# Performance work log

Hardware: AMD Instinct MI355X
Metric: run time of the kernel (lower is better)

The kernel has to match this reference:

```python
import jax, jax.numpy as jnp
import numpy as np
import math

D_MODEL = 1024
N_HEADS = 8
HEAD_DIM = D_MODEL // N_HEADS
N_CLASSES = 2


def setup_inputs() -> dict:
    key = jax.random.key(0)
    ks = jax.random.split(key, 12)
    s = 1.0 / math.sqrt(D_MODEL)
    return {
        "x": jax.random.normal(ks[0], (8192, D_MODEL), dtype=jnp.float32),
        "class_token": jax.random.normal(ks[1], (1, 1, D_MODEL), dtype=jnp.float32),
        "Wq": jax.random.normal(ks[2], (D_MODEL, D_MODEL), dtype=jnp.float32) * s,
        "bq": jnp.zeros((D_MODEL,), jnp.float32),
        "Wk": jax.random.normal(ks[3], (D_MODEL, D_MODEL), dtype=jnp.float32) * s,
        "bk": jnp.zeros((D_MODEL,), jnp.float32),
        "Wv": jax.random.normal(ks[4], (D_MODEL, D_MODEL), dtype=jnp.float32) * s,
        "bv": jnp.zeros((D_MODEL,), jnp.float32),
        "Wo": jax.random.normal(ks[5], (D_MODEL, D_MODEL), dtype=jnp.float32) * s,
        "bo": jnp.zeros((D_MODEL,), jnp.float32),
        "Wc": jax.random.normal(ks[6], (N_CLASSES, D_MODEL), dtype=jnp.float32) * s,
        "bc": jnp.zeros((N_CLASSES,), jnp.float32),
    }


def reference(x, class_token, Wq, bq, Wk, bk, Wv, bv, Wo, bo, Wc, bc):
    # Prepend class token: [T, D] with T = N_patches + 1 (batch size is 1)
    tokens = jnp.concatenate([class_token.reshape(1, D_MODEL), x], axis=0)
    T = tokens.shape[0]
    scale = 1.0 / math.sqrt(HEAD_DIM)

    def heads(W, b):
        return (tokens @ W.T + b).reshape(T, N_HEADS, HEAD_DIM).transpose(1, 0, 2)

    q = heads(Wq, bq)  # [H, T, hd]
    k = heads(Wk, bk)
    v = heads(Wv, bv)

    scores = jnp.einsum("htd,hsd->hts", q, k) * scale  # [H, T, T]
    probs = jax.nn.softmax(scores, axis=-1)
    attn_out = jnp.einsum("hts,hsd->htd", probs, v)  # [H, T, hd]

    # MIL attention weights: class-token row, over patches, head-averaged
    A = probs[:, 0, 1:].mean(axis=0)[None, :]  # [1, N_patches]

    out = attn_out.transpose(1, 0, 2).reshape(T, D_MODEL) @ Wo.T + bo  # [T, D]
    cls_out = out[0:1]  # [1, D]

    logits = cls_out @ Wc.T + bc  # [1, n_classes]
    y_probs = jax.nn.softmax(logits, axis=1)

    m = jnp.argmax(y_probs.reshape(-1))
    row = m // N_CLASSES
    Y_hat = (m % N_CLASSES)[None]  # [1]
    top_instance = jnp.take(logits, row, axis=0)[None]  # [1, n_classes]
    Y_prob = jnp.take(y_probs, row, axis=0)[None]  # [1, n_classes]

    return top_instance, Y_prob, Y_hat, y_probs, A
```

## Files before the change

### kernel.cpp

```cpp
#include <hip/hip_runtime.h>
#include <math.h>

#define D 1024
#define NH 8
#define T 8193

#define OFF_LOGITS 0
#define OFF_DONE   2
#define OFF_E      4
#define OFF_G      2052
#define OFF_W      18436
#define ZERO_FLTS  26628
#define OFF_QCLS   26628
#define OFF_CH     27652
#define OFF_CONST  27660
#define OFF_L      27664
#define OFF_SCT    29712
#define OFF_UB     95256

static __device__ __forceinline__ float wred(float v) {
    #pragma unroll
    for (int m = 32; m; m >>= 1) v += __shfl_xor(v, m, 64);
    return v;
}

#define DPPADD(v, ctrl) \
    ((v) + __int_as_float(__builtin_amdgcn_update_dpp( \
        0, __float_as_int(v), (ctrl), 0xf, 0xf, true)))

static __device__ __forceinline__ float wave_total(float v) {
    v = DPPADD(v, 0x111);
    v = DPPADD(v, 0x112);
    v = DPPADD(v, 0x114);
    v = DPPADD(v, 0x118);
    v = DPPADD(v, 0x142);
    v = DPPADD(v, 0x143);
    return __int_as_float(__builtin_amdgcn_readlane(__float_as_int(v), 63));
}

__global__ __launch_bounds__(256) void k1(const float* __restrict__ Wq,
                                          const float* __restrict__ bq,
                                          const float* __restrict__ ct,
                                          const float* __restrict__ Wc,
                                          const float* __restrict__ Wo,
                                          float* __restrict__ ws) {
    __shared__ float red[4];
    int b = blockIdx.x, t = threadIdx.x;
    if (b < 1024) {
        const float4* wr = (const float4*)(Wq + (size_t)b * D);
        const float4* cv = (const float4*)ct;
        float4 a = wr[t], c = cv[t];
        float v = a.x*c.x + a.y*c.y + a.z*c.z + a.w*c.w;
        v = wred(v);
        if ((t & 63) == 0) red[t >> 6] = v;
        __syncthreads();
        if (t == 0) ws[OFF_QCLS + b] = red[0]+red[1]+red[2]+red[3] + bq[b];
    } else {
        int idx = b - 1024;
        int c = idx >> 5, i0 = (idx & 31) * 32;
        const float4* Wo4 = (const float4*)Wo;
        float4 acc = {0,0,0,0};
        #pragma unroll 8
        for (int i = 0; i < 32; ++i) {
            float s = Wc[c * D + i0 + i];
            float4 r = Wo4[(size_t)(i0 + i) * 256 + t];
            acc.x += s*r.x; acc.y += s*r.y; acc.z += s*r.z; acc.w += s*r.w;
        }
        float* e = ws + OFF_E + c * D + t * 4;
        atomicAdd(e+0, acc.x); atomicAdd(e+1, acc.y);
        atomicAdd(e+2, acc.z); atomicAdd(e+3, acc.w);
    }
}

__global__ __launch_bounds__(1024) void k2(const float* __restrict__ Wk,
                                           const float* __restrict__ bk,
                                           const float* __restrict__ Wv,
                                           const float* __restrict__ Wc,
                                           const float* __restrict__ bo,
                                           const float* __restrict__ bv,
                                           const float* __restrict__ bc,
                                           float* __restrict__ ws) {
    int b = blockIdx.x, t = threadIdx.x;
    int w = t >> 6, lane = t & 63;
    if (b < 64) {
        int h = b >> 3, seg = b & 7;
        float acc = 0.f;
        const float* base = Wk + ((size_t)(h*128 + seg*16)) * D + t;
        #pragma unroll
        for (int d = 0; d < 16; ++d)
            acc += ws[OFF_QCLS + h*128 + seg*16 + d] * base[(size_t)d * D];
        atomicAdd(&ws[OFF_W + h*D + t], acc);
    } else if (b < 192) {
        __shared__ float4 gred[4][256];
        int idx = b - 64;
        int c = idx >> 6, h = (idx >> 3) & 7, rseg = idx & 7;
        int j4 = t & 255, rsub = t >> 8;
        int r0 = h*128 + rseg*16 + rsub*4;
        const float4* Wv4 = (const float4*)Wv;
        float4 acc = {0,0,0,0};
        #pragma unroll
        for (int r = 0; r < 4; ++r) {
            float s = ws[OFF_E + c*D + r0 + r];
            float4 v = Wv4[(size_t)(r0 + r) * 256 + j4];
            acc.x += s*v.x; acc.y += s*v.y; acc.z += s*v.z; acc.w += s*v.w;
        }
        gred[rsub][j4] = acc;
        __syncthreads();
        if (rsub == 0) {
            float4 a0 = gred[0][j4], a1 = gred[1][j4], a2 = gred[2][j4], a3 = gred[3][j4];
            float* g = ws + OFF_G + c*8192 + h*D + j4*4;
            atomicAdd(g+0, a0.x+a1.x+a2.x+a3.x);
            atomicAdd(g+1, a0.y+a1.y+a2.y+a3.y);
            atomicAdd(g+2, a0.z+a1.z+a2.z+a3.z);
            atomicAdd(g+3, a0.w+a1.w+a2.w+a3.w);
        }
    } else if (b == 192) {
        __shared__ float red[16];
        int h = t >> 7, d = t & 127;
        float v = ws[OFF_QCLS + h*128 + d] * bk[h*128 + d];
        v = wred(v);
        if (lane == 0) red[w] = v;
        __syncthreads();
        if (t < 8) ws[OFF_CH + t] = red[2*t] + red[2*t+1];
    } else {
        __shared__ float red[32];
        float v0 = Wc[t]*bo[t] + ws[OFF_E + t]*bv[t];
        float v1 = Wc[D + t]*bo[t] + ws[OFF_E + D + t]*bv[t];
        v0 = wred(v0); v1 = wred(v1);
        if (lane == 0) { red[w] = v0; red[16 + w] = v1; }
        __syncthreads();
        if (t == 0) {
            float a0 = 0.f, a1 = 0.f;
            #pragma unroll
            for (int i = 0; i < 16; ++i) { a0 += red[i]; a1 += red[16+i]; }
            ws[OFF_CONST + 0] = a0 + bc[0];
            ws[OFF_CONST + 1] = a1 + bc[1];
        }
    }
}

__global__ __launch_bounds__(512, 2) void k3(const float* __restrict__ x,
                                             const float* __restrict__ ct,
                                             float* __restrict__ ws) {
    __shared__ float stash[33 * D];
    __shared__ float pe[33][8];
    const int b = blockIdx.x, t = threadIdx.x;
    const int w = t >> 6, lane = t & 63;

    float4 wreg[8][4];
    const float4* wg4 = (const float4*)(ws + OFF_W);
    #pragma unroll
    for (int h = 0; h < 8; ++h) {
        #pragma unroll
        for (int j = 0; j < 4; ++j)
            wreg[h][j] = wg4[h * 256 + j * 64 + lane];
    }
    float chv[8];
    #pragma unroll
    for (int h = 0; h < 8; ++h) chv[h] = ws[OFF_CH + h];

    const int ntok_blk = (b == 255) ? 33 : 32;
    const int ntok_w   = (b == 255 && w == 7) ? 5 : 4;
    for (int i = 0; i < ntok_w; ++i) {
        int k = w * 4 + i;
        int s = b * 32 + k;
        const float* row = (s == 0) ? ct : (x + (size_t)(s - 1) * D);
        float* dst = stash + k * D;
        #pragma unroll
        for (int q = 0; q < 4; ++q)
            __builtin_amdgcn_global_load_lds(
                (const __attribute__((address_space(1))) unsigned int*)(row + q * 256 + lane * 4),
                (__attribute__((address_space(3))) unsigned int*)(dst + q * 256),
                16, 0, 0);
    }
    __builtin_amdgcn_s_waitcnt(0x0f70);

    const float scale = 0.08838834764831845f;
    for (int i = 0; i < ntok_w; ++i) {
        int k = w * 4 + i;
        int s = b * 32 + k;
        const float4* tk = (const float4*)(stash + k * D);
        float4 t0 = tk[lane], t1 = tk[64 + lane], t2 = tk[128 + lane], t3 = tk[192 + lane];
        float sc[8];
        #pragma unroll
        for (int h = 0; h < 8; ++h) {
            float4 w0 = wreg[h][0], w1 = wreg[h][1], w2 = wreg[h][2], w3 = wreg[h][3];
            float v = w0.x*t0.x + w0.y*t0.y + w0.z*t0.z + w0.w*t0.w
                    + w1.x*t1.x + w1.y*t1.y + w1.z*t1.z + w1.w*t1.w
                    + w2.x*t2.x + w2.y*t2.y + w2.z*t2.z + w2.w*t2.w
                    + w3.x*t3.x + w3.y*t3.y + w3.z*t3.z + w3.w*t3.w;
            v = wave_total(v);
            sc[h] = scale * (v + chv[h]);
        }
        if (lane == 0) {
            float4* sct = (float4*)(ws + OFF_SCT);
            sct[s * 2]     = make_float4(sc[0], sc[1], sc[2], sc[3]);
            sct[s * 2 + 1] = make_float4(sc[4], sc[5], sc[6], sc[7]);
            *(float4*)&pe[k][0] = make_float4(__expf(sc[0]), __expf(sc[1]),
                                              __expf(sc[2]), __expf(sc[3]));
            *(float4*)&pe[k][4] = make_float4(__expf(sc[4]), __expf(sc[5]),
                                              __expf(sc[6]), __expf(sc[7]));
        }
    }
    __syncthreads();

    if (t < 8) {
        float s = 0.f;
        for (int k = 0; k < ntok_blk; ++k) s += pe[k][t];
        ws[OFF_L + b * 8 + t] = s;
    }

    const int f4 = t & 255, half = t >> 8;
    const float4* st4 = (const float4*)stash;
    float4 acc0 = {0,0,0,0}, acc1 = {0,0,0,0}, acc2 = {0,0,0,0}, acc3 = {0,0,0,0};
    for (int k = 0; k < ntok_blk; ++k) {
        float4 tv = st4[k * 256 + f4];
        float4 pv = *(const float4*)&pe[k][half * 4];
        acc0.x += pv.x*tv.x; acc0.y += pv.x*tv.y; acc0.z += pv.x*tv.z; acc0.w += pv.x*tv.w;
        acc1.x += pv.y*tv.x; acc1.y += pv.y*tv.y; acc1.z += pv.y*tv.z; acc1.w += pv.y*tv.w;
        acc2.x += pv.z*tv.x; acc2.y += pv.z*tv.y; acc2.z += pv.z*tv.z; acc2.w += pv.z*tv.w;
        acc3.x += pv.w*tv.x; acc3.y += pv.w*tv.y; acc3.z += pv.w*tv.z; acc3.w += pv.w*tv.w;
    }
    float4* ub4 = (float4*)(ws + OFF_UB) + (size_t)b * 2048;
    ub4[(half*4 + 0) * 256 + f4] = acc0;
    ub4[(half*4 + 1) * 256 + f4] = acc1;
    ub4[(half*4 + 2) * 256 + f4] = acc2;
    ub4[(half*4 + 3) * 256 + f4] = acc3;
}

__global__ __launch_bounds__(1024) void k4(float* __restrict__ out,
                                           float* __restrict__ ws) {
    __shared__ float red[32][33];
    __shared__ float lp[8][9];
    __shared__ float rlh[8];
    __shared__ float a0r[32], a1r[32];
    const int b = blockIdx.x, t = threadIdx.x;

    if (t < 64) {
        int h = t & 7, seg = t >> 3;
        float s = 0.f;
        for (int pb = seg * 32; pb < seg * 32 + 32; ++pb) s += ws[OFF_L + pb * 8 + h];
        lp[seg][h] = s;
    }
    __syncthreads();
    if (t < 8) {
        float s = 0.f;
        #pragma unroll
        for (int i = 0; i < 8; ++i) s += lp[i][t];
        rlh[t] = 1.f / s;
    }
    __syncthreads();

    {
        int seg = t >> 5, j = t & 31;
        float acc = 0.f;
        for (int pb = seg * 8; pb < seg * 8 + 8; ++pb)
            acc += ws[OFF_UB + (size_t)pb * 8192 + b * 32 + j];
        red[seg][j] = acc;
    }
    __syncthreads();
    if (t < 32) {
        float uval = 0.f;
        #pragma unroll
        for (int i = 0; i < 32; ++i) uval += red[i][t];
        uval *= rlh[b >> 5];
        int jg = b * 32 + t;
        a0r[t] = ws[OFF_G + jg] * uval;
        a1r[t] = ws[OFF_G + 8192 + jg] * uval;
    }
    if (t >= 64 && t < 96) {
        int s = b * 32 + 1 + (t - 64);
        const float4* sct = (const float4*)(ws + OFF_SCT);
        float4 sa = sct[s * 2], sb = sct[s * 2 + 1];
        float sum = __expf(sa.x)*rlh[0] + __expf(sa.y)*rlh[1]
                  + __expf(sa.z)*rlh[2] + __expf(sa.w)*rlh[3]
                  + __expf(sb.x)*rlh[4] + __expf(sb.y)*rlh[5]
                  + __expf(sb.z)*rlh[6] + __expf(sb.w)*rlh[7];
        out[6 + s] = sum * 0.125f;
    }
    __syncthreads();
    if (t == 0) {
        float v0 = 0.f, v1 = 0.f;
        #pragma unroll
        for (int i = 0; i < 32; ++i) { v0 += a0r[i]; v1 += a1r[i]; }
        atomicAdd(&ws[OFF_LOGITS + 0], v0);
        atomicAdd(&ws[OFF_LOGITS + 1], v1);
        __threadfence();
        unsigned old = atomicAdd((unsigned*)(ws + OFF_DONE), 1u);
        if (old == 255) {
            float l0 = atomicAdd(&ws[OFF_LOGITS + 0], 0.f) + ws[OFF_CONST + 0];
            float l1 = atomicAdd(&ws[OFF_LOGITS + 1], 0.f) + ws[OFF_CONST + 1];
            float mx = fmaxf(l0, l1);
            float e0 = __expf(l0 - mx), e1 = __expf(l1 - mx);
            float inv = 1.f / (e0 + e1);
            float p0 = e0 * inv, p1 = e1 * inv;
            int am = (p1 > p0) ? 1 : 0;
            out[0] = l0; out[1] = l1;
            out[2] = p0; out[3] = p1;
            out[4] = (float)am;
            out[5] = p0; out[6] = p1;
        }
    }
}

extern "C" void kernel_launch(void* const* d_in, const int* in_sizes, int n_in,
                              void* d_out, int out_size, void* d_ws, size_t ws_size,
                              hipStream_t stream) {
    const float* x  = (const float*)d_in[0];
    const float* ct = (const float*)d_in[1];
    const float* Wq = (const float*)d_in[2];
    const float* bq = (const float*)d_in[3];
    const float* Wk = (const float*)d_in[4];
    const float* bk = (const float*)d_in[5];
    const float* Wv = (const float*)d_in[6];
    const float* bv = (const float*)d_in[7];
    const float* Wo = (const float*)d_in[8];
    const float* bo = (const float*)d_in[9];
    const float* Wc = (const float*)d_in[10];
    const float* bc = (const float*)d_in[11];
    float* out = (float*)d_out;
    float* ws  = (float*)d_ws;

    hipMemsetAsync(d_ws, 0, ZERO_FLTS * sizeof(float), stream);
    k1<<<dim3(1088), dim3(256),  0, stream>>>(Wq, bq, ct, Wc, Wo, ws);
    k2<<<dim3(194),  dim3(1024), 0, stream>>>(Wk, bk, Wv, Wc, bo, bv, bc, ws);
    k3<<<dim3(256),  dim3(512),  0, stream>>>(x, ct, ws);
    k4<<<dim3(256),  dim3(1024), 0, stream>>>(out, ws);
}
```

Measured before the change: 135.9 us.

## Remove atomics and memset, fold logit projection into k3, pipeline token loads

Replaces atomic accumulation in k1/k2 with per-block partial buffers reduced deterministically, which removes the workspace memset launch. The G-projection of the per-block attention-weighted sums now happens inside k3, so only small per-block logit partials are written instead of the large UB buffer that k4 had to re-read. k3 waits on each token's async LDS load separately so compute can overlap the remaining loads, and it stores exponentiated scores so k4 skips the exp. The costs are a bit more register pressure in k3 and a serial reduction in one k4 block.

New measurement: 125.1 us. 1.09x faster.

```diff
diff --git a/kernel.cpp b/kernel.cpp
--- a/kernel.cpp
+++ b/kernel.cpp
@@ -5,18 +5,15 @@
 #define NH 8
 #define T 8193
 
-#define OFF_LOGITS 0
-#define OFF_DONE   2
-#define OFF_E      4
-#define OFF_G      2052
-#define OFF_W      18436
-#define ZERO_FLTS  26628
-#define OFF_QCLS   26628
-#define OFF_CH     27652
-#define OFF_CONST  27660
-#define OFF_L      27664
-#define OFF_SCT    29712
-#define OFF_UB     95256
+#define OFF_QCLS  0
+#define OFF_EP    1024
+#define OFF_W     17408
+#define OFF_G     25600
+#define OFF_CH    41984
+#define OFF_CONST 41992
+#define OFF_L     42000
+#define OFF_PLOG  44048
+#define OFF_SCT   48144
 
 static __device__ __forceinline__ float wred(float v) {
     #pragma unroll
@@ -38,37 +35,50 @@
     return __int_as_float(__builtin_amdgcn_readlane(__float_as_int(v), 63));
 }
 
-__global__ __launch_bounds__(256) void k1(const float* __restrict__ Wq,
-                                          const float* __restrict__ bq,
-                                          const float* __restrict__ ct,
-                                          const float* __restrict__ Wc,
-                                          const float* __restrict__ Wo,
-                                          float* __restrict__ ws) {
-    __shared__ float red[4];
-    int b = blockIdx.x, t = threadIdx.x;
-    if (b < 1024) {
-        const float4* wr = (const float4*)(Wq + (size_t)b * D);
+__global__ __launch_bounds__(1024) void k1(const float* __restrict__ Wq,
+                                           const float* __restrict__ bq,
+                                           const float* __restrict__ ct,
+                                           const float* __restrict__ Wc,
+                                           const float* __restrict__ Wo,
+                                           float* __restrict__ ws) {
+    __shared__ float red[16];
+    __shared__ float er[4][2][256];
+    const int b = blockIdx.x, t = threadIdx.x;
+    const int w = t >> 6, lane = t & 63;
+    if (b < 256) {
+        int grp = t >> 8, f4 = t & 255;
+        int r = b * 4 + grp;
+        const float4* wr = (const float4*)(Wq + (size_t)r * D);
         const float4* cv = (const float4*)ct;
-        float4 a = wr[t], c = cv[t];
+        float4 a = wr[f4], c = cv[f4];
         float v = a.x*c.x + a.y*c.y + a.z*c.z + a.w*c.w;
         v = wred(v);
-        if ((t & 63) == 0) red[t >> 6] = v;
-        __syncthreads();
-        if (t == 0) ws[OFF_QCLS + b] = red[0]+red[1]+red[2]+red[3] + bq[b];
+        if (lane == 0) red[w] = v;
+        __syncthreads();
+        if (t < 4)
+            ws[OFF_QCLS + b*4 + t] = red[4*t]+red[4*t+1]+red[4*t+2]+red[4*t+3] + bq[b*4 + t];
     } else {
-        int idx = b - 1024;
-        int c = idx >> 5, i0 = (idx & 31) * 32;
-        const float4* Wo4 = (const float4*)Wo;
-        float4 acc = {0,0,0,0};
+        int idx = b - 256;
+        int p = idx >> 2, jq = idx & 3;
+        int layer = t >> 8, jl = t & 255;
+        int j = jq * 256 + jl;
+        int i0 = p * 128 + layer * 32;
+        const float* wo = Wo + (size_t)i0 * D + j;
+        float a0 = 0.f, a1 = 0.f;
         #pragma unroll 8
         for (int i = 0; i < 32; ++i) {
-            float s = Wc[c * D + i0 + i];
-            float4 r = Wo4[(size_t)(i0 + i) * 256 + t];
-            acc.x += s*r.x; acc.y += s*r.y; acc.z += s*r.z; acc.w += s*r.w;
-        }
-        float* e = ws + OFF_E + c * D + t * 4;
-        atomicAdd(e+0, acc.x); atomicAdd(e+1, acc.y);
-        atomicAdd(e+2, acc.z); atomicAdd(e+3, acc.w);
+            float r = wo[(size_t)i * D];
+            a0 += Wc[i0 + i] * r;
+            a1 += Wc[D + i0 + i] * r;
+        }
+        er[layer][0][jl] = a0;
+        er[layer][1][jl] = a1;
+        __syncthreads();
+        if (t < 512) {
+            int c = t >> 8, jl2 = t & 255;
+            ws[OFF_EP + p*2048 + c*1024 + jq*256 + jl2] =
+                er[0][c][jl2] + er[1][c][jl2] + er[2][c][jl2] + er[3][c][jl2];
+        }
     }
 }
 
@@ -80,42 +90,55 @@
                                            const float* __restrict__ bv,
                                            const float* __restrict__ bc,
                                            float* __restrict__ ws) {
-    int b = blockIdx.x, t = threadIdx.x;
-    int w = t >> 6, lane = t & 63;
-    if (b < 64) {
-        int h = b >> 3, seg = b & 7;
+    __shared__ float qh[128];
+    __shared__ float el[2][128];
+    __shared__ float lr[4][2][256];
+    __shared__ float red[32];
+    const int b = blockIdx.x, t = threadIdx.x;
+    const int w = t >> 6, lane = t & 63;
+    if (b < 32) {
+        int h = b >> 2, jq = b & 3;
+        if (t < 128) qh[t] = ws[OFF_QCLS + h*128 + t];
+        __syncthreads();
+        int layer = t >> 8, jl = t & 255;
+        int j = jq * 256 + jl, d0 = layer * 32;
+        const float* wk = Wk + (size_t)(h*128 + d0) * D + j;
         float acc = 0.f;
-        const float* base = Wk + ((size_t)(h*128 + seg*16)) * D + t;
-        #pragma unroll
-        for (int d = 0; d < 16; ++d)
-            acc += ws[OFF_QCLS + h*128 + seg*16 + d] * base[(size_t)d * D];
-        atomicAdd(&ws[OFF_W + h*D + t], acc);
-    } else if (b < 192) {
-        __shared__ float4 gred[4][256];
-        int idx = b - 64;
-        int c = idx >> 6, h = (idx >> 3) & 7, rseg = idx & 7;
-        int j4 = t & 255, rsub = t >> 8;
-        int r0 = h*128 + rseg*16 + rsub*4;
-        const float4* Wv4 = (const float4*)Wv;
-        float4 acc = {0,0,0,0};
-        #pragma unroll
-        for (int r = 0; r < 4; ++r) {
-            float s = ws[OFF_E + c*D + r0 + r];
-            float4 v = Wv4[(size_t)(r0 + r) * 256 + j4];
-            acc.x += s*v.x; acc.y += s*v.y; acc.z += s*v.z; acc.w += s*v.w;
-        }
-        gred[rsub][j4] = acc;
-        __syncthreads();
-        if (rsub == 0) {
-            float4 a0 = gred[0][j4], a1 = gred[1][j4], a2 = gred[2][j4], a3 = gred[3][j4];
-            float* g = ws + OFF_G + c*8192 + h*D + j4*4;
-            atomicAdd(g+0, a0.x+a1.x+a2.x+a3.x);
-            atomicAdd(g+1, a0.y+a1.y+a2.y+a3.y);
-            atomicAdd(g+2, a0.z+a1.z+a2.z+a3.z);
-            atomicAdd(g+3, a0.w+a1.w+a2.w+a3.w);
-        }
-    } else if (b == 192) {
-        __shared__ float red[16];
+        #pragma unroll 8
+        for (int d = 0; d < 32; ++d) acc += qh[d0 + d] * wk[(size_t)d * D];
+        lr[layer][0][jl] = acc;
+        __syncthreads();
+        if (t < 256)
+            ws[OFF_W + h*1024 + jq*256 + t] = lr[0][0][t]+lr[1][0][t]+lr[2][0][t]+lr[3][0][t];
+    } else if (b < 64) {
+        int hb = b - 32, h = hb >> 2, jq = hb & 3;
+        if (t < 256) {
+            int c = t >> 7, r = t & 127;
+            float s = 0.f;
+            #pragma unroll
+            for (int p = 0; p < 8; ++p) s += ws[OFF_EP + p*2048 + c*1024 + h*128 + r];
+            el[c][r] = s;
+        }
+        __syncthreads();
+        int layer = t >> 8, jl = t & 255;
+        int j = jq * 256 + jl, r0 = layer * 32;
+        const float* wv = Wv + (size_t)(h*128 + r0) * D + j;
+        float a0 = 0.f, a1 = 0.f;
+        #pragma unroll 8
+        for (int r = 0; r < 32; ++r) {
+            float xv = wv[(size_t)r * D];
+            a0 += el[0][r0 + r] * xv;
+            a1 += el[1][r0 + r] * xv;
+        }
+        lr[layer][0][jl] = a0;
+        lr[layer][1][jl] = a1;
+        __syncthreads();
+        if (t < 512) {
+            int c = t >> 8, jl2 = t & 255;
+            ws[OFF_G + c*8192 + h*1024 + jq*256 + jl2] =
+                lr[0][c][jl2] + lr[1][c][jl2] + lr[2][c][jl2] + lr[3][c][jl2];
+        }
+    } else if (b == 64) {
         int h = t >> 7, d = t & 127;
         float v = ws[OFF_QCLS + h*128 + d] * bk[h*128 + d];
         v = wred(v);
@@ -123,16 +146,21 @@
         __syncthreads();
         if (t < 8) ws[OFF_CH + t] = red[2*t] + red[2*t+1];
     } else {
-        __shared__ float red[32];
-        float v0 = Wc[t]*bo[t] + ws[OFF_E + t]*bv[t];
-        float v1 = Wc[D + t]*bo[t] + ws[OFF_E + D + t]*bv[t];
+        float e0 = 0.f, e1 = 0.f;
+        #pragma unroll
+        for (int p = 0; p < 8; ++p) {
+            e0 += ws[OFF_EP + p*2048 + t];
+            e1 += ws[OFF_EP + p*2048 + 1024 + t];
+        }
+        float v0 = Wc[t]*bo[t] + e0*bv[t];
+        float v1 = Wc[D + t]*bo[t] + e1*bv[t];
         v0 = wred(v0); v1 = wred(v1);
         if (lane == 0) { red[w] = v0; red[16 + w] = v1; }
         __syncthreads();
         if (t == 0) {
             float a0 = 0.f, a1 = 0.f;
             #pragma unroll
-            for (int i = 0; i < 16; ++i) { a0 += red[i]; a1 += red[16+i]; }
+            for (int i = 0; i < 16; ++i) { a0 += red[i]; a1 += red[16 + i]; }
             ws[OFF_CONST + 0] = a0 + bc[0];
             ws[OFF_CONST + 1] = a1 + bc[1];
         }
@@ -144,25 +172,26 @@
                                              float* __restrict__ ws) {
     __shared__ float stash[33 * D];
     __shared__ float pe[33][8];
+    __shared__ float plred[8][8];
     const int b = blockIdx.x, t = threadIdx.x;
     const int w = t >> 6, lane = t & 63;
 
     float4 wreg[8][4];
     const float4* wg4 = (const float4*)(ws + OFF_W);
     #pragma unroll
-    for (int h = 0; h < 8; ++h) {
+    for (int h = 0; h < 8; ++h)
         #pragma unroll
         for (int j = 0; j < 4; ++j)
             wreg[h][j] = wg4[h * 256 + j * 64 + lane];
-    }
     float chv[8];
     #pragma unroll
     for (int h = 0; h < 8; ++h) chv[h] = ws[OFF_CH + h];
 
     const int ntok_blk = (b == 255) ? 33 : 32;
-    const int ntok_w   = (b == 255 && w == 7) ? 5 : 4;
+    const bool tail = (b == 255 && w == 7);
+    const int ntok_w = tail ? 5 : 4;
     for (int i = 0; i < ntok_w; ++i) {
-        int k = w * 4 + i;
+        int k = (i < 4) ? (w * 4 + i) : 32;
         int s = b * 32 + k;
         const float* row = (s == 0) ? ct : (x + (size_t)(s - 1) * D);
         float* dst = stash + k * D;
@@ -173,15 +202,13 @@
                 (__attribute__((address_space(3))) unsigned int*)(dst + q * 256),
                 16, 0, 0);
     }
-    __builtin_amdgcn_s_waitcnt(0x0f70);
 
     const float scale = 0.08838834764831845f;
-    for (int i = 0; i < ntok_w; ++i) {
-        int k = w * 4 + i;
+    auto compute = [&](int k) {
         int s = b * 32 + k;
         const float4* tk = (const float4*)(stash + k * D);
         float4 t0 = tk[lane], t1 = tk[64 + lane], t2 = tk[128 + lane], t3 = tk[192 + lane];
-        float sc[8];
+        float pv[8];
         #pragma unroll
         for (int h = 0; h < 8; ++h) {
             float4 w0 = wreg[h][0], w1 = wreg[h][1], w2 = wreg[h][2], w3 = wreg[h][3];
@@ -190,17 +217,25 @@
                     + w2.x*t2.x + w2.y*t2.y + w2.z*t2.z + w2.w*t2.w
                     + w3.x*t3.x + w3.y*t3.y + w3.z*t3.z + w3.w*t3.w;
             v = wave_total(v);
-            sc[h] = scale * (v + chv[h]);
+            pv[h] = __expf(scale * (v + chv[h]));
         }
         if (lane == 0) {
             float4* sct = (float4*)(ws + OFF_SCT);
-            sct[s * 2]     = make_float4(sc[0], sc[1], sc[2], sc[3]);
-            sct[s * 2 + 1] = make_float4(sc[4], sc[5], sc[6], sc[7]);
-            *(float4*)&pe[k][0] = make_float4(__expf(sc[0]), __expf(sc[1]),
-                                              __expf(sc[2]), __expf(sc[3]));
-            *(float4*)&pe[k][4] = make_float4(__expf(sc[4]), __expf(sc[5]),
-                                              __expf(sc[6]), __expf(sc[7]));
-        }
+            sct[s * 2]     = make_float4(pv[0], pv[1], pv[2], pv[3]);
+            sct[s * 2 + 1] = make_float4(pv[4], pv[5], pv[6], pv[7]);
+            *(float4*)&pe[k][0] = make_float4(pv[0], pv[1], pv[2], pv[3]);
+            *(float4*)&pe[k][4] = make_float4(pv[4], pv[5], pv[6], pv[7]);
+        }
+    };
+
+    if (!tail) {
+        __builtin_amdgcn_s_waitcnt(0x0f7c); compute(w*4 + 0);
+        __builtin_amdgcn_s_waitcnt(0x0f78); compute(w*4 + 1);
+        __builtin_amdgcn_s_waitcnt(0x0f74); compute(w*4 + 2);
+        __builtin_amdgcn_s_waitcnt(0x0f70); compute(w*4 + 3);
+    } else {
+        __builtin_amdgcn_s_waitcnt(0x0f70);
+        for (int i = 0; i < 5; ++i) compute((i < 4) ? (w*4 + i) : 32);
     }
     __syncthreads();
 
@@ -221,75 +256,79 @@
         acc2.x += pv.z*tv.x; acc2.y += pv.z*tv.y; acc2.z += pv.z*tv.z; acc2.w += pv.z*tv.w;
         acc3.x += pv.w*tv.x; acc3.y += pv.w*tv.y; acc3.z += pv.w*tv.z; acc3.w += pv.w*tv.w;
     }
-    float4* ub4 = (float4*)(ws + OFF_UB) + (size_t)b * 2048;
-    ub4[(half*4 + 0) * 256 + f4] = acc0;
-    ub4[(half*4 + 1) * 256 + f4] = acc1;
-    ub4[(half*4 + 2) * 256 + f4] = acc2;
-    ub4[(half*4 + 3) * 256 + f4] = acc3;
-}
-
-__global__ __launch_bounds__(1024) void k4(float* __restrict__ out,
-                                           float* __restrict__ ws) {
-    __shared__ float red[32][33];
-    __shared__ float lp[8][9];
+
+    const float4* G4 = (const float4*)(ws + OFF_G);
+    float pl[8];
+    #pragma unroll
+    for (int c = 0; c < 2; ++c) {
+        float4 g0 = G4[c*2048 + (half*4 + 0)*256 + f4];
+        float4 g1 = G4[c*2048 + (half*4 + 1)*256 + f4];
+        float4 g2 = G4[c*2048 + (half*4 + 2)*256 + f4];
+        float4 g3 = G4[c*2048 + (half*4 + 3)*256 + f4];
+        pl[c*4+0] = g0.x*acc0.x + g0.y*acc0.y + g0.z*acc0.z + g0.w*acc0.w;
+        pl[c*4+1] = g1.x*acc1.x + g1.y*acc1.y + g1.z*acc1.z + g1.w*acc1.w;
+        pl[c*4+2] = g2.x*acc2.x + g2.y*acc2.y + g2.z*acc2.z + g2.w*acc2.w;
+        pl[c*4+3] = g3.x*acc3.x + g3.y*acc3.y + g3.z*acc3.z + g3.w*acc3.w;
+    }
+    #pragma unroll
+    for (int v = 0; v < 8; ++v) pl[v] = wave_total(pl[v]);
+    if (lane == 0)
+        #pragma unroll
+        for (int v = 0; v < 8; ++v) plred[w][v] = pl[v];
+    __syncthreads();
+    if (t < 16) {
+        int c = t >> 3, hh = t & 7;
+        int wb = (hh < 4) ? 0 : 4, vi = c * 4 + (hh & 3);
+        ws[OFF_PLOG + b*16 + t] =
+            plred[wb][vi] + plred[wb+1][vi] + plred[wb+2][vi] + plred[wb+3][vi];
+    }
+}
+
+__global__ __launch_bounds__(256) void k4(float* __restrict__ out,
+                                          float* __restrict__ ws) {
+    __shared__ float lp[32][8];
     __shared__ float rlh[8];
-    __shared__ float a0r[32], a1r[32];
+    __shared__ float r2[8];
     const int b = blockIdx.x, t = threadIdx.x;
 
-    if (t < 64) {
-        int h = t & 7, seg = t >> 3;
+    {
+        int seg = t >> 3, h = t & 7;
         float s = 0.f;
-        for (int pb = seg * 32; pb < seg * 32 + 32; ++pb) s += ws[OFF_L + pb * 8 + h];
+        for (int pb = seg; pb < 256; pb += 32) s += ws[OFF_L + pb*8 + h];
         lp[seg][h] = s;
     }
     __syncthreads();
     if (t < 8) {
         float s = 0.f;
         #pragma unroll
-        for (int i = 0; i < 8; ++i) s += lp[i][t];
+        for (int i = 0; i < 32; ++i) s += lp[i][t];
         rlh[t] = 1.f / s;
     }
     __syncthreads();
 
-    {
-        int seg = t >> 5, j = t & 31;
-        float acc = 0.f;
-        for (int pb = seg * 8; pb < seg * 8 + 8; ++pb)
-            acc += ws[OFF_UB + (size_t)pb * 8192 + b * 32 + j];
-        red[seg][j] = acc;
-    }
-    __syncthreads();
     if (t < 32) {
-        float uval = 0.f;
-        #pragma unroll
-        for (int i = 0; i < 32; ++i) uval += red[i][t];
-        uval *= rlh[b >> 5];
-        int jg = b * 32 + t;
-        a0r[t] = ws[OFF_G + jg] * uval;
-        a1r[t] = ws[OFF_G + 8192 + jg] * uval;
-    }
-    if (t >= 64 && t < 96) {
-        int s = b * 32 + 1 + (t - 64);
+        int s_ = b * 32 + t + 1;
         const float4* sct = (const float4*)(ws + OFF_SCT);
-        float4 sa = sct[s * 2], sb = sct[s * 2 + 1];
-        float sum = __expf(sa.x)*rlh[0] + __expf(sa.y)*rlh[1]
-                  + __expf(sa.z)*rlh[2] + __expf(sa.w)*rlh[3]
-                  + __expf(sb.x)*rlh[4] + __expf(sb.y)*rlh[5]
-                  + __expf(sb.z)*rlh[6] + __expf(sb.w)*rlh[7];
-        out[6 + s] = sum * 0.125f;
-    }
-    __syncthreads();
-    if (t == 0) {
+        float4 pa = sct[s_ * 2], pb4 = sct[s_ * 2 + 1];
+        float sum = pa.x*rlh[0] + pa.y*rlh[1] + pa.z*rlh[2] + pa.w*rlh[3]
+                  + pb4.x*rlh[4] + pb4.y*rlh[5] + pb4.z*rlh[6] + pb4.w*rlh[7];
+        out[6 + s_] = sum * 0.125f;
+    }
+
+    if (b == 0) {
         float v0 = 0.f, v1 = 0.f;
-        #pragma unroll
-        for (int i = 0; i < 32; ++i) { v0 += a0r[i]; v1 += a1r[i]; }
-        atomicAdd(&ws[OFF_LOGITS + 0], v0);
-        atomicAdd(&ws[OFF_LOGITS + 1], v1);
-        __threadfence();
-        unsigned old = atomicAdd((unsigned*)(ws + OFF_DONE), 1u);
-        if (old == 255) {
-            float l0 = atomicAdd(&ws[OFF_LOGITS + 0], 0.f) + ws[OFF_CONST + 0];
-            float l1 = atomicAdd(&ws[OFF_LOGITS + 1], 0.f) + ws[OFF_CONST + 1];
+        for (int idx = t; idx < 4096; idx += 256) {
+            float val = ws[OFF_PLOG + idx];
+            int rem = idx & 15;
+            float z = val * rlh[rem & 7];
+            if ((rem >> 3) == 0) v0 += z; else v1 += z;
+        }
+        v0 = wred(v0); v1 = wred(v1);
+        if ((t & 63) == 0) { r2[t >> 6] = v0; r2[4 + (t >> 6)] = v1; }
+        __syncthreads();
+        if (t == 0) {
+            float l0 = r2[0]+r2[1]+r2[2]+r2[3] + ws[OFF_CONST + 0];
+            float l1 = r2[4]+r2[5]+r2[6]+r2[7] + ws[OFF_CONST + 1];
             float mx = fmaxf(l0, l1);
             float e0 = __expf(l0 - mx), e1 = __expf(l1 - mx);
             float inv = 1.f / (e0 + e1);
@@ -321,9 +360,8 @@
     float* out = (float*)d_out;
     float* ws  = (float*)d_ws;
 
-    hipMemsetAsync(d_ws, 0, ZERO_FLTS * sizeof(float), stream);
-    k1<<<dim3(1088), dim3(256),  0, stream>>>(Wq, bq, ct, Wc, Wo, ws);
-    k2<<<dim3(194),  dim3(1024), 0, stream>>>(Wk, bk, Wv, Wc, bo, bv, bc, ws);
-    k3<<<dim3(256),  dim3(512),  0, stream>>>(x, ct, ws);
-    k4<<<dim3(256),  dim3(1024), 0, stream>>>(out, ws);
-}
+    k1<<<dim3(288), dim3(1024), 0, stream>>>(Wq, bq, ct, Wc, Wo, ws);
+    k2<<<dim3(66),  dim3(1024), 0, stream>>>(Wk, bk, Wv, Wc, bo, bv, bc, ws);
+    k3<<<dim3(256), dim3(512),  0, stream>>>(x, ct, ws);
+    k4<<<dim3(256), dim3(256),  0, stream>>>(out, ws);
+}
```
